# Optimization experiments

Measured on AMD Instinct MI355X. Metric: run time of the kernel, lower is better.

## Reference

```python
import jax, jax.numpy as jnp
import numpy as np
from jax import lax

# Fixed-point format: Q*.8 (8 fractional bits), as used by HGRNFixed8bit's
# to_fixed/from_fixed round-trip. We simulate it in float via round(x*256)/256.
FRAC = 256.0
EPS = 1e-5
B, T, D = 4, 2048, 2048  # batch, seq_len, hidden_size; input_dim = D (expand_ratio=1)


def to_fixed(x):
    return jnp.round(x * FRAC) / FRAC


def to_ternary(w):
    # BitNet-style ternarization: sign(w/mean|w|), zeroed where |w_norm| < 0.5
    scale = jnp.mean(jnp.abs(w))
    wn = w / (scale + 1e-5)
    t = jnp.sign(wn)
    return jnp.where(jnp.abs(wn) < 0.5, 0.0, t).astype(jnp.float32)


def per_channel_scale(w):
    # compute_scale: mean |w| over dim 0, stored in fixed point
    return to_fixed(jnp.mean(jnp.abs(w), axis=0))


def setup_inputs() -> dict:
    key = jax.random.key(0)
    ks = jax.random.split(key, 6)
    hidden_states = jax.random.normal(ks[0], (B, T, D), dtype=jnp.float32)
    # float master weights, then quantize exactly as quantize_weights() does
    w_i_f = jax.random.normal(ks[1], (D, D), dtype=jnp.float32) * 0.02  # i_proj.weight.T
    w_f_f = jax.random.normal(ks[2], (D, D), dtype=jnp.float32) * 0.02  # f_proj.weight.T
    w_g_f = jax.random.normal(ks[3], (D, D), dtype=jnp.float32) * 0.02  # g_proj.weight.T
    w_o_f = jax.random.normal(ks[4], (D, D), dtype=jnp.float32) * 0.02  # o_proj.weight [D_out, D_in]
    g_norm_w = jnp.ones((D,), dtype=jnp.float32)  # g_norm (RMSNorm-swish-gate) weight
    return {
        "hidden_states": hidden_states,
        "w_i": to_ternary(w_i_f), "w_f": to_ternary(w_f_f),
        "w_g": to_ternary(w_g_f), "w_o": to_ternary(w_o_f),
        "s_i": per_channel_scale(w_i_f), "s_f": per_channel_scale(w_f_f),
        "s_g": per_channel_scale(w_g_f), "s_o": per_channel_scale(w_o_f),
        "g_norm_w": g_norm_w,
    }


def reference(hidden_states, w_i, w_f, w_g, w_o, s_i, s_f, s_g, s_o, g_norm_w):
    # Quantize activations to 8-bit fixed point (to_fixed)
    x = to_fixed(hidden_states)                       # [B,T,D]
    # Ternary dequant-matmuls with per-channel scales
    i = jnp.einsum('btd,de->bte', x, w_i) * s_i       # input branch
    f = jax.nn.sigmoid(jnp.einsum('btd,de->bte', x, w_f) * s_f)  # forget gate
    g = jnp.einsum('btd,de->bte', x, w_g) * s_g       # output gate
    i = (1.0 - f) * i                                 # HGRN input gating
    # Gated linear recurrence h_t = f_t * h_{t-1} + i_t via associative scan
    def combine(a, b):
        af, ai = a
        bf, bi = b
        return (af * bf, ai * bf + bi)
    _, h = lax.associative_scan(combine, (f, i), axis=1)  # [B,T,E]
    # FusedRMSNormSwishGate: rmsnorm(h) * weight * swish(g)
    rms = h * lax.rsqrt(jnp.mean(h * h, axis=-1, keepdims=True) + EPS)
    o = rms * g_norm_w * (g * jax.nn.sigmoid(g))
    # Output ternary matmul (o_proj, weight untransposed -> use w_o.T),
    # per-input-channel scale, then from_fixed round-trip of the fixed output
    out = to_fixed(jnp.einsum('bte,oe->bto', o * s_o, w_o))  # [B,T,D]
    return out
```

## Files before the change

### kernel.cpp

```cpp
#include <hip/hip_runtime.h>
#include <hip/hip_bf16.h>
#include <stdint.h>
#include <math.h>


#define BATCH 4
#define SEQ   2048
#define DIM   2048
#define MROWS (BATCH*SEQ)
#define TCH   64
#define NCH   (SEQ/TCH)

#define GBM 256
#define GBN 256
#define GBK 64
#define GNT (DIM/GBK)
#define HALF 8192
#define SLOT (4*HALF)

typedef unsigned short u16;
typedef __attribute__((ext_vector_type(8))) short short8;
typedef __attribute__((ext_vector_type(4))) float f32x4;

static __device__ __forceinline__ u16 f2bf_rne(float x) {
  uint32_t u = __float_as_uint(x);
  u += 0x7FFFu + ((u >> 16) & 1u);
  return (u16)(u >> 16);
}
static __device__ __forceinline__ float bf2f(u16 h) {
  return __uint_as_float(((uint32_t)h) << 16);
}

static __device__ __forceinline__ void gl2lds16(const void* g, void* l) {
  __builtin_amdgcn_global_load_lds((const __attribute__((address_space(1))) void*)g,
                                   (__attribute__((address_space(3))) void*)l,
                                   16, 0, 0);
}

__global__ __launch_bounds__(256) void diag_ws(float* __restrict__ out, float val) {
  size_t i = ((size_t)blockIdx.x * 256 + threadIdx.x) * 8;
#pragma unroll
  for (int j = 0; j < 8; j++) out[i + j] = val;
}

__global__ __launch_bounds__(256) void prep_x(const float* __restrict__ x,
                                              u16* __restrict__ XB) {
  size_t i = ((size_t)blockIdx.x * 256 + threadIdx.x) * 4;
  float4 v = *(const float4*)(x + i);
  float q[4] = {v.x, v.y, v.z, v.w};
  u16 hh[4];
#pragma unroll
  for (int j = 0; j < 4; j++) {
    float xq = rintf(q[j] * 256.0f) * 0.00390625f;
    hh[j] = f2bf_rne(xq);
  }
  *(uint2*)(XB + i) = make_uint2((uint32_t)hh[0] | ((uint32_t)hh[1] << 16),
                                 (uint32_t)hh[2] | ((uint32_t)hh[3] << 16));
}

__global__ void prep_wT(const float* __restrict__ w_i, const float* __restrict__ w_f,
                        const float* __restrict__ w_g, u16* __restrict__ WT) {
  __shared__ u16 tile[32][33];
  const int g = blockIdx.z;
  const float* __restrict__ w = (g == 0) ? w_i : (g == 1) ? w_f : w_g;
  u16* __restrict__ outp = WT + (size_t)g * DIM * DIM;
  const int d0 = blockIdx.x * 32;
  const int e0 = blockIdx.y * 32;
  const int tx = threadIdx.x;
  const int ty = threadIdx.y;
  for (int ii = ty; ii < 32; ii += 8)
    tile[ii][tx] = f2bf_rne(w[(size_t)(d0 + ii) * DIM + e0 + tx]);
  __syncthreads();
  for (int ii = ty; ii < 32; ii += 8)
    outp[(size_t)(e0 + ii) * DIM + d0 + tx] = tile[tx][ii];
}

__global__ __launch_bounds__(256) void prep_wo(const float* __restrict__ w, u16* __restrict__ WB) {
  size_t i = ((size_t)blockIdx.x * 256 + threadIdx.x) * 4;
  float4 v = *(const float4*)(w + i);
  *(uint2*)(WB + i) = make_uint2((uint32_t)f2bf_rne(v.x) | ((uint32_t)f2bf_rne(v.y) << 16),
                                 (uint32_t)f2bf_rne(v.z) | ((uint32_t)f2bf_rne(v.w) << 16));
}

static __device__ __forceinline__ void stage_half(const u16* g, u16* l, int tid) {
  gl2lds16(g, l + (size_t)tid * 8);
  gl2lds16(g + (size_t)64 * DIM, l + (size_t)(tid + 512) * 8);
}

static __device__ __forceinline__ void kloop256(const u16* __restrict__ Ag,
                                                const u16* __restrict__ Bg,
                                                u16* lds, f32x4 (&acc)[8][4]) {
  const int tid = threadIdx.x;
  const int lane16 = tid & 15;
  const int quad = (tid & 63) >> 4;
  const int wid = tid >> 6;
  const int wR = wid >> 2;
  const int wC = wid & 3;

  const int rowS = tid >> 3;
  const int ccS = ((tid & 7) ^ (rowS & 7)) * 8;
  const u16* gA = Ag + (size_t)rowS * DIM + ccS;
  const u16* gB = Bg + (size_t)rowS * DIM + ccS;
  const size_t gH = (size_t)128 * DIM;

  const int cswz = lane16 & 7;
  const int ck0 = (quad ^ cswz) * 8;
  const int ck1 = ((4 + quad) ^ cswz) * 8;
  const int arow = (wR * 64 + lane16) * 64;
  const int brow = (wC * 32 + lane16) * 64;

  stage_half(gA,      lds + 0 * HALF, tid);
  stage_half(gB,      lds + 2 * HALF, tid);
  stage_half(gB + gH, lds + 3 * HALF, tid);
  stage_half(gA + gH, lds + 1 * HALF, tid);
  asm volatile("s_waitcnt vmcnt(2)" ::: "memory");
  __builtin_amdgcn_s_barrier();

  short8 af[4][2], bfr[4][2];

#pragma unroll 1
  for (int t = 0; t < GNT; ++t) {
    const u16* S = lds + (t & 1) * SLOT;
    u16* SN = lds + ((t + 1) & 1) * SLOT;
    const bool pf = (t + 1 < GNT);
    const size_t tg = (size_t)(t + 1) * GBK;

#pragma unroll
    for (int j = 0; j < 4; j++) {
      const u16* bb = S + 2 * HALF + (j >> 1) * HALF + brow + (j & 1) * 1024;
      bfr[j][0] = *(const short8*)(bb + ck0);
      bfr[j][1] = *(const short8*)(bb + ck1);
    }
#pragma unroll
    for (int mi = 0; mi < 4; mi++) {
      const u16* aa = S + arow + mi * 1024;
      af[mi][0] = *(const short8*)(aa + ck0);
      af[mi][1] = *(const short8*)(aa + ck1);
    }
    if (pf) {
      stage_half(gA + tg, SN + 0 * HALF, tid);
      stage_half(gB + tg, SN + 2 * HALF, tid);
      asm volatile("s_waitcnt vmcnt(4)" ::: "memory");
    } else {
      asm volatile("s_waitcnt vmcnt(0)" ::: "memory");
    }
    __builtin_amdgcn_s_barrier();
    __builtin_amdgcn_s_setprio(1);
#pragma unroll
    for (int mi = 0; mi < 4; mi++)
#pragma unroll
      for (int j = 0; j < 4; j++) {
        acc[mi][j] = __builtin_amdgcn_mfma_f32_16x16x32_bf16(af[mi][0], bfr[j][0], acc[mi][j], 0, 0, 0);
        acc[mi][j] = __builtin_amdgcn_mfma_f32_16x16x32_bf16(af[mi][1], bfr[j][1], acc[mi][j], 0, 0, 0);
      }
    __builtin_amdgcn_s_setprio(0);

#pragma unroll
    for (int mi = 0; mi < 4; mi++) {
      const u16* aa = S + HALF + arow + mi * 1024;
      af[mi][0] = *(const short8*)(aa + ck0);
      af[mi][1] = *(const short8*)(aa + ck1);
    }
    if (pf) {
      stage_half(gB + gH + tg, SN + 3 * HALF, tid);
      stage_half(gA + gH + tg, SN + 1 * HALF, tid);
      asm volatile("s_waitcnt vmcnt(2)" ::: "memory");
      __builtin_amdgcn_s_barrier();
    }
    __builtin_amdgcn_s_setprio(1);
#pragma unroll
    for (int mi = 0; mi < 4; mi++)
#pragma unroll
      for (int j = 0; j < 4; j++) {
        acc[4 + mi][j] = __builtin_amdgcn_mfma_f32_16x16x32_bf16(af[mi][0], bfr[j][0], acc[4 + mi][j], 0, 0, 0);
        acc[4 + mi][j] = __builtin_amdgcn_mfma_f32_16x16x32_bf16(af[mi][1], bfr[j][1], acc[4 + mi][j], 0, 0, 0);
      }
    __builtin_amdgcn_s_setprio(0);
  }
}

__global__ __launch_bounds__(512, 2) void gemm_gates8(
    const u16* __restrict__ XB, const u16* __restrict__ WT,
    const float* __restrict__ s_i, const float* __restrict__ s_f, const float* __restrict__ s_g,
    const float* __restrict__ gnw, const float* __restrict__ s_o,
    u16* __restrict__ Ib, u16* __restrict__ Fb, u16* __restrict__ Gb) {
  __shared__ __align__(16) u16 lds[2 * SLOT];
  const int bid = blockIdx.x;
  const int i = (bid & 7) * 96 + (bid >> 3);
  const int gate = i >> 8;
  const int r = i & 255;
  const int sr = r >> 5;
  const int s = r & 31;
  const int m0 = (sr * 4 + (s & 3)) * GBM;
  const int n0 = (s >> 2) * GBN;

  const u16* Ag = XB + (size_t)m0 * DIM;
  const u16* Bg = WT + (size_t)gate * DIM * DIM + (size_t)n0 * DIM;

  f32x4 acc[8][4];
#pragma unroll
  for (int a = 0; a < 8; a++)
#pragma unroll
    for (int b = 0; b < 4; b++) acc[a][b] = {0.f, 0.f, 0.f, 0.f};

  kloop256(Ag, Bg, lds, acc);

  __syncthreads();
  const int tid = threadIdx.x;
  const int lane16 = tid & 15;
  const int quad = (tid & 63) >> 4;
  const int wid = tid >> 6;
  const int wR = wid >> 2;
  const int wC = wid & 3;
  const float* __restrict__ sc = (gate == 0) ? s_i : (gate == 1) ? s_f : s_g;
  u16* __restrict__ Out = (gate == 0) ? Ib : (gate == 1) ? Fb : Gb;
  u16* T = lds;
#pragma unroll
  for (int p = 0; p < 2; ++p) {
#pragma unroll
    for (int ni = 0; ni < 2; ++ni) {
      const int tcol = wC * 32 + ni * 16 + lane16;
      const int n = n0 + p * 128 + tcol;
      const float scale = sc[n];
      const float post = (gate == 2) ? gnw[n] * s_o[n] : 0.f;
#pragma unroll
      for (int hA = 0; hA < 2; ++hA)
#pragma unroll
        for (int mi = 0; mi < 4; ++mi) {
          const int lrow = hA * 128 + wR * 64 + mi * 16 + quad * 4;
#pragma unroll
          for (int r2 = 0; r2 < 4; ++r2) {
            float v = acc[hA * 4 + mi][p * 2 + ni][r2] * scale;
            if (gate == 1) v = 1.0f / (1.0f + expf(-v));
            if (gate == 2) v = v / (1.0f + expf(-v)) * post;
            T[(lrow + r2) * 136 + tcol] = f2bf_rne(v);
          }
        }
    }
    __syncthreads();
#pragma unroll
    for (int j = 0; j < 8; j++) {
      const int id = tid + j * 512;
      const int row = id >> 4;
      const int c16 = id & 15;
      uint4 v = *(const uint4*)(T + row * 136 + c16 * 8);
      *(uint4*)(Out + (size_t)(m0 + row) * DIM + n0 + p * 128 + c16 * 8) = v;
    }
    __syncthreads();
  }
}

__global__ __launch_bounds__(512, 2) void gemm_out8(const u16* __restrict__ OS,
                                                    const u16* __restrict__ WOB,
                                                    float* __restrict__ out) {
  __shared__ __align__(16) u16 lds[2 * SLOT];
  const int bid = blockIdx.x;
  const int l = bid >> 3;
  const int m0 = ((bid & 7) * 4 + (l & 3)) * GBM;
  const int n0 = (l >> 2) * GBN;

  const u16* Ag = OS + (size_t)m0 * DIM;
  const u16* Bg = WOB + (size_t)n0 * DIM;

  f32x4 acc[8][4];
#pragma unroll
  for (int a = 0; a < 8; a++)
#pragma unroll
    for (int b = 0; b < 4; b++) acc[a][b] = {0.f, 0.f, 0.f, 0.f};

  kloop256(Ag, Bg, lds, acc);

  const int tid = threadIdx.x;
  const int lane16 = tid & 15;
  const int quad = (tid & 63) >> 4;
  const int wid = tid >> 6;
  const int wR = wid >> 2;
  const int wC = wid & 3;
#pragma unroll
  for (int p = 0; p < 2; ++p)
#pragma unroll
    for (int ni = 0; ni < 2; ++ni) {
      const int n = n0 + p * 128 + wC * 32 + ni * 16 + lane16;
#pragma unroll
      for (int hA = 0; hA < 2; ++hA)
#pragma unroll
        for (int mi = 0; mi < 4; ++mi) {
          const int mrow = m0 + hA * 128 + wR * 64 + mi * 16 + quad * 4;
#pragma unroll
          for (int r2 = 0; r2 < 4; ++r2)
            out[(size_t)(mrow + r2) * DIM + n] =
                rintf(acc[hA * 4 + mi][p * 2 + ni][r2] * 256.0f) * 0.00390625f;
        }
    }
}

__global__ __launch_bounds__(256) void scan_phase1(const u16* __restrict__ Fb,
                                                   const u16* __restrict__ Ib,
                                                   float* __restrict__ Pc,
                                                   float* __restrict__ Sc) {
  const int e0 = (blockIdx.x * 256 + threadIdx.x) * 2;
  const int c = blockIdx.y;
  const int b = blockIdx.z;
  const size_t base = ((size_t)b * SEQ + (size_t)c * TCH) * DIM + e0;
  float P0 = 1.f, S0 = 0.f, P1 = 1.f, S1 = 0.f;
  for (int t = 0; t < TCH; t++) {
    const uint32_t fp = *(const uint32_t*)(Fb + base + (size_t)t * DIM);
    const uint32_t ip = *(const uint32_t*)(Ib + base + (size_t)t * DIM);
    const float f0 = bf2f((u16)fp), f1 = bf2f((u16)(fp >> 16));
    const float i0 = bf2f((u16)ip), i1 = bf2f((u16)(ip >> 16));
    S0 = S0 * f0 + (1.f - f0) * i0;  P0 *= f0;
    S1 = S1 * f1 + (1.f - f1) * i1;  P1 *= f1;
  }
  const size_t ci = ((size_t)b * NCH + c) * DIM + e0;
  *(float2*)(Pc + ci) = make_float2(P0, P1);
  *(float2*)(Sc + ci) = make_float2(S0, S1);
}

__global__ __launch_bounds__(256) void scan_phase2(const u16* __restrict__ Fb,
                                                   const u16* __restrict__ Ib,
                                                   const float* __restrict__ Pc,
                                                   const float* __restrict__ Sc,
                                                   u16* __restrict__ Hb) {
  const int e0 = (blockIdx.x * 256 + threadIdx.x) * 2;
  const int c = blockIdx.y;
  const int b = blockIdx.z;
  float h0 = 0.f, h1 = 0.f;
  for (int cc = 0; cc < c; cc++) {
    const size_t ci = ((size_t)b * NCH + cc) * DIM + e0;
    const float2 p = *(const float2*)(Pc + ci);
    const float2 s = *(const float2*)(Sc + ci);
    h0 = s.x + p.x * h0;
    h1 = s.y + p.y * h1;
  }
  const size_t base = ((size_t)b * SEQ + (size_t)c * TCH) * DIM + e0;
  for (int t = 0; t < TCH; t++) {
    const uint32_t fp = *(const uint32_t*)(Fb + base + (size_t)t * DIM);
    const uint32_t ip = *(const uint32_t*)(Ib + base + (size_t)t * DIM);
    const float f0 = bf2f((u16)fp), f1 = bf2f((u16)(fp >> 16));
    const float i0 = bf2f((u16)ip), i1 = bf2f((u16)(ip >> 16));
    h0 = f0 * h0 + (1.f - f0) * i0;
    h1 = f1 * h1 + (1.f - f1) * i1;
    *(uint32_t*)(Hb + base + (size_t)t * DIM) =
        (uint32_t)f2bf_rne(h0) | ((uint32_t)f2bf_rne(h1) << 16);
  }
}

__global__ __launch_bounds__(256) void rms_gate(const u16* __restrict__ Hb,
                                                const u16* __restrict__ SwGb,
                                                u16* __restrict__ OS) {
  const size_t base = (size_t)blockIdx.x * DIM;
  const int tid = threadIdx.x;
  const int e0 = tid * 8;
  uint4 hp = *(const uint4*)(Hb + base + e0);
  float hv[8];
  hv[0] = bf2f((u16)hp.x); hv[1] = bf2f((u16)(hp.x >> 16));
  hv[2] = bf2f((u16)hp.y); hv[3] = bf2f((u16)(hp.y >> 16));
  hv[4] = bf2f((u16)hp.z); hv[5] = bf2f((u16)(hp.z >> 16));
  hv[6] = bf2f((u16)hp.w); hv[7] = bf2f((u16)(hp.w >> 16));
  float ss = 0.f;
#pragma unroll
  for (int j = 0; j < 8; j++) ss += hv[j] * hv[j];
#pragma unroll
  for (int off = 32; off > 0; off >>= 1) ss += __shfl_down(ss, off, 64);
  __shared__ float red[4];
  if ((tid & 63) == 0) red[tid >> 6] = ss;
  __syncthreads();
  const float tot = red[0] + red[1] + red[2] + red[3];
  const float inv = 1.0f / sqrtf(tot * (1.0f / (float)DIM) + 1e-5f);

  uint4 gp = *(const uint4*)(SwGb + base + e0);
  float gv[8];
  gv[0] = bf2f((u16)gp.x); gv[1] = bf2f((u16)(gp.x >> 16));
  gv[2] = bf2f((u16)gp.y); gv[3] = bf2f((u16)(gp.y >> 16));
  gv[4] = bf2f((u16)gp.z); gv[5] = bf2f((u16)(gp.z >> 16));
  gv[6] = bf2f((u16)gp.w); gv[7] = bf2f((u16)(gp.w >> 16));
  u16 ov[8];
#pragma unroll
  for (int j = 0; j < 8; j++) ov[j] = f2bf_rne(hv[j] * inv * gv[j]);
  uint4 op;
  op.x = (uint32_t)ov[0] | ((uint32_t)ov[1] << 16);
  op.y = (uint32_t)ov[2] | ((uint32_t)ov[3] << 16);
  op.z = (uint32_t)ov[4] | ((uint32_t)ov[5] << 16);
  op.w = (uint32_t)ov[6] | ((uint32_t)ov[7] << 16);
  *(uint4*)(OS + base + e0) = op;
}

extern "C" void kernel_launch(void* const* d_in, const int* in_sizes, int n_in,
                              void* d_out, int out_size, void* d_ws, size_t ws_size,
                              hipStream_t stream) {
  (void)in_sizes; (void)n_in; (void)out_size;
  const float* x   = (const float*)d_in[0];
  const float* w_i = (const float*)d_in[1];
  const float* w_f = (const float*)d_in[2];
  const float* w_g = (const float*)d_in[3];
  const float* w_o = (const float*)d_in[4];
  const float* s_i = (const float*)d_in[5];
  const float* s_f = (const float*)d_in[6];
  const float* s_g = (const float*)d_in[7];
  const float* s_o = (const float*)d_in[8];
  const float* gnw = (const float*)d_in[9];
  float* out = (float*)d_out;

  const size_t MB = 1024 * 1024;
  const size_t NEED = 88 * MB;
  if (ws_size < NEED) {
    diag_ws<<<MROWS * DIM / 2048, 256, 0, stream>>>(out, (float)(ws_size / MB));
    return;
  }

  uint8_t* ws = (uint8_t*)d_ws;
  u16* XB = (u16*)(ws);
  u16* WT = (u16*)(ws + 32 * MB);
  u16* Ib = (u16*)(ws + 56 * MB);
  float* Pc = (float*)(ws + 32 * MB);
  float* Sc = (float*)(ws + 33 * MB);
  u16* WOB = (u16*)(ws + 34 * MB);
  u16* Hb  = XB;
  u16* OS  = Ib;
  u16* Gb = (u16*)d_out;
  u16* Fb = (u16*)((uint8_t*)d_out + 32 * MB);

  prep_x<<<MROWS * DIM / 1024, 256, 0, stream>>>(x, XB);
  prep_wT<<<dim3(DIM / 32, DIM / 32, 3), dim3(32, 8, 1), 0, stream>>>(w_i, w_f, w_g, WT);
  gemm_gates8<<<768, 512, 0, stream>>>(XB, WT, s_i, s_f, s_g, gnw, s_o, Ib, Fb, Gb);
  scan_phase1<<<dim3(DIM / 512, NCH, BATCH), 256, 0, stream>>>(Fb, Ib, Pc, Sc);
  scan_phase2<<<dim3(DIM / 512, NCH, BATCH), 256, 0, stream>>>(Fb, Ib, Pc, Sc, Hb);
  prep_wo<<<DIM * DIM / 1024, 256, 0, stream>>>(w_o, WOB);
  rms_gate<<<MROWS, 256, 0, stream>>>(Hb, Gb, OS);
  gemm_out8<<<256, 512, 0, stream>>>(OS, WOB, out);
}
```

Baseline: 512.2 us.

## Split GEMM k-step into four quadrant phases with finer-grained prefetch waits

Restructures the double-buffered bf16 MFMA main loop from two phases into four. The B fragments are split into low and high halves, and each quadrant of the 256x256 tile is computed in its own phase, with one global-to-LDS half-tile stage issued per phase. This lowers live B-fragment registers and spreads the global loads more evenly across the MFMA work, so memory latency can hide behind compute. In exchange it adds more barriers per k-step, and the vmcnt accounting becomes more delicate.

```diff
diff --git a/kernel.cpp b/kernel.cpp
--- a/kernel.cpp
+++ b/kernel.cpp
@@ -113,10 +113,10 @@
   stage_half(gB,      lds + 2 * HALF, tid);
   stage_half(gB + gH, lds + 3 * HALF, tid);
   stage_half(gA + gH, lds + 1 * HALF, tid);
-  asm volatile("s_waitcnt vmcnt(2)" ::: "memory");
+  asm volatile("s_waitcnt vmcnt(4)" ::: "memory");
   __builtin_amdgcn_s_barrier();
 
-  short8 af[4][2], bfr[4][2];
+  short8 af[4][2], bl[2][2], bh[2][2];
 
 #pragma unroll 1
   for (int t = 0; t < GNT; ++t) {
@@ -126,34 +126,52 @@
     const size_t tg = (size_t)(t + 1) * GBK;
 
 #pragma unroll
-    for (int j = 0; j < 4; j++) {
-      const u16* bb = S + 2 * HALF + (j >> 1) * HALF + brow + (j & 1) * 1024;
-      bfr[j][0] = *(const short8*)(bb + ck0);
-      bfr[j][1] = *(const short8*)(bb + ck1);
-    }
-#pragma unroll
     for (int mi = 0; mi < 4; mi++) {
       const u16* aa = S + arow + mi * 1024;
       af[mi][0] = *(const short8*)(aa + ck0);
       af[mi][1] = *(const short8*)(aa + ck1);
     }
-    if (pf) {
-      stage_half(gA + tg, SN + 0 * HALF, tid);
-      stage_half(gB + tg, SN + 2 * HALF, tid);
-      asm volatile("s_waitcnt vmcnt(4)" ::: "memory");
-    } else {
-      asm volatile("s_waitcnt vmcnt(0)" ::: "memory");
-    }
+#pragma unroll
+    for (int ni = 0; ni < 2; ni++) {
+      const u16* bb = S + 2 * HALF + brow + ni * 1024;
+      bl[ni][0] = *(const short8*)(bb + ck0);
+      bl[ni][1] = *(const short8*)(bb + ck1);
+    }
+    if (pf) stage_half(gA + tg, SN + 0 * HALF, tid);
     __builtin_amdgcn_s_barrier();
     __builtin_amdgcn_s_setprio(1);
 #pragma unroll
     for (int mi = 0; mi < 4; mi++)
 #pragma unroll
-      for (int j = 0; j < 4; j++) {
-        acc[mi][j] = __builtin_amdgcn_mfma_f32_16x16x32_bf16(af[mi][0], bfr[j][0], acc[mi][j], 0, 0, 0);
-        acc[mi][j] = __builtin_amdgcn_mfma_f32_16x16x32_bf16(af[mi][1], bfr[j][1], acc[mi][j], 0, 0, 0);
+      for (int ni = 0; ni < 2; ni++) {
+        acc[mi][ni] = __builtin_amdgcn_mfma_f32_16x16x32_bf16(af[mi][0], bl[ni][0], acc[mi][ni], 0, 0, 0);
+        acc[mi][ni] = __builtin_amdgcn_mfma_f32_16x16x32_bf16(af[mi][1], bl[ni][1], acc[mi][ni], 0, 0, 0);
       }
     __builtin_amdgcn_s_setprio(0);
+    if (pf) { asm volatile("s_waitcnt vmcnt(4)" ::: "memory"); }
+    else    { asm volatile("s_waitcnt vmcnt(2)" ::: "memory"); }
+    __builtin_amdgcn_s_barrier();
+
+#pragma unroll
+    for (int ni = 0; ni < 2; ni++) {
+      const u16* bb = S + 3 * HALF + brow + ni * 1024;
+      bh[ni][0] = *(const short8*)(bb + ck0);
+      bh[ni][1] = *(const short8*)(bb + ck1);
+    }
+    if (pf) stage_half(gB + tg, SN + 2 * HALF, tid);
+    __builtin_amdgcn_s_barrier();
+    __builtin_amdgcn_s_setprio(1);
+#pragma unroll
+    for (int mi = 0; mi < 4; mi++)
+#pragma unroll
+      for (int ni = 0; ni < 2; ni++) {
+        acc[mi][2 + ni] = __builtin_amdgcn_mfma_f32_16x16x32_bf16(af[mi][0], bh[ni][0], acc[mi][2 + ni], 0, 0, 0);
+        acc[mi][2 + ni] = __builtin_amdgcn_mfma_f32_16x16x32_bf16(af[mi][1], bh[ni][1], acc[mi][2 + ni], 0, 0, 0);
+      }
+    __builtin_amdgcn_s_setprio(0);
+    if (pf) { asm volatile("s_waitcnt vmcnt(4)" ::: "memory"); }
+    else    { asm volatile("s_waitcnt vmcnt(0)" ::: "memory"); }
+    __builtin_amdgcn_s_barrier();
 
 #pragma unroll
     for (int mi = 0; mi < 4; mi++) {
@@ -161,21 +179,32 @@
       af[mi][0] = *(const short8*)(aa + ck0);
       af[mi][1] = *(const short8*)(aa + ck1);
     }
-    if (pf) {
-      stage_half(gB + gH + tg, SN + 3 * HALF, tid);
-      stage_half(gA + gH + tg, SN + 1 * HALF, tid);
-      asm volatile("s_waitcnt vmcnt(2)" ::: "memory");
-      __builtin_amdgcn_s_barrier();
-    }
+    if (pf) stage_half(gB + gH + tg, SN + 3 * HALF, tid);
+    __builtin_amdgcn_s_barrier();
     __builtin_amdgcn_s_setprio(1);
 #pragma unroll
     for (int mi = 0; mi < 4; mi++)
 #pragma unroll
-      for (int j = 0; j < 4; j++) {
-        acc[4 + mi][j] = __builtin_amdgcn_mfma_f32_16x16x32_bf16(af[mi][0], bfr[j][0], acc[4 + mi][j], 0, 0, 0);
-        acc[4 + mi][j] = __builtin_amdgcn_mfma_f32_16x16x32_bf16(af[mi][1], bfr[j][1], acc[4 + mi][j], 0, 0, 0);
+      for (int ni = 0; ni < 2; ni++) {
+        acc[4 + mi][ni] = __builtin_amdgcn_mfma_f32_16x16x32_bf16(af[mi][0], bl[ni][0], acc[4 + mi][ni], 0, 0, 0);
+        acc[4 + mi][ni] = __builtin_amdgcn_mfma_f32_16x16x32_bf16(af[mi][1], bl[ni][1], acc[4 + mi][ni], 0, 0, 0);
       }
     __builtin_amdgcn_s_setprio(0);
+    __builtin_amdgcn_s_barrier();
+
+    if (pf) stage_half(gA + gH + tg, SN + 1 * HALF, tid);
+    __builtin_amdgcn_s_barrier();
+    __builtin_amdgcn_s_setprio(1);
+#pragma unroll
+    for (int mi = 0; mi < 4; mi++)
+#pragma unroll
+      for (int ni = 0; ni < 2; ni++) {
+        acc[4 + mi][2 + ni] = __builtin_amdgcn_mfma_f32_16x16x32_bf16(af[mi][0], bh[ni][0], acc[4 + mi][2 + ni], 0, 0, 0);
+        acc[4 + mi][2 + ni] = __builtin_amdgcn_mfma_f32_16x16x32_bf16(af[mi][1], bh[ni][1], acc[4 + mi][2 + ni], 0, 0, 0);
+      }
+    __builtin_amdgcn_s_setprio(0);
+    if (pf) { asm volatile("s_waitcnt vmcnt(4)" ::: "memory"); }
+    __builtin_amdgcn_s_barrier();
   }
 }
 
```

Result: no change. 507.4 us (-0.9%).
